# Optimization experiments

Measured on AMD Instinct MI355X. Metric: run time of the kernel, lower is better.

## Reference

```python
import jax, jax.numpy as jnp
import numpy as np

EPS = 1e-6  # AngularPhysicsConfig.eps


def setup_inputs() -> dict:
    key = jax.random.key(0)
    k1, k2 = jax.random.split(key)
    B, L, d, H = 2, 2048, 2048, 8
    x_spatial = jax.random.normal(k1, (B, L, d), dtype=jnp.float32)
    # attn is a softmax output: rows sum to 1 over the last axis
    attn = jax.nn.softmax(jax.random.normal(k2, (B, H, L, L), dtype=jnp.float32), axis=-1)
    W = jnp.ones((1,), dtype=jnp.float32)   # nn.Parameter(torch.ones(1))
    b = jnp.zeros((1,), dtype=jnp.float32)  # bias_init = 0.0
    return {"x_spatial": x_spatial, "attn": attn, "W": W, "b": b}


def reference(x_spatial, attn, W, b):
    # --- angular_kernel ---
    norm = jnp.clip(jnp.linalg.norm(x_spatial, axis=-1, keepdims=True), EPS, None)
    x_unit = x_spatial / norm                                   # [B, L, d]
    K = jnp.einsum('bld,bmd->blm', x_unit, x_unit)              # [B, L, L] cosine sim
    K_mean = K.mean(axis=(-1, -2), keepdims=True)
    K_cent = K - K_mean
    # torch .std() is unbiased (ddof=1), computed on detached K_cent
    K_std = jnp.std(jax.lax.stop_gradient(K_cent), axis=(-1, -2), keepdims=True, ddof=1)
    K_norm = K_cent / jnp.clip(K_std, EPS, None)                # [B, L, L]

    # --- compute_cos_align (detach_attn_for_alignment=True) ---
    A = jax.lax.stop_gradient(attn.mean(axis=1))                # [B, L, L]
    cos_align = jnp.sum(A * K_norm, axis=-1)                    # [B, L]

    # --- gate ---
    gate = jax.nn.sigmoid(W * cos_align + b)                    # [B, L]
    return gate, cos_align, K_norm
```

## Files before the change

### kernel.cpp

```cpp
#include <hip/hip_runtime.h>
#include <hip/hip_bf16.h>

#define L_DIM 2048
#define D_DIM 2048
#define B_DIM 2
#define H_DIM 8
#define NT 16
#define NPAIR 136
#define NRED 512
#define NKT (D_DIM / 64)
#define EPSV 1e-6f

using bf16x8 = __attribute__((ext_vector_type(8))) __bf16;
using f32x4  = __attribute__((ext_vector_type(4))) float;
using f4     = __attribute__((ext_vector_type(4))) float;

__device__ inline void gload_lds16(const void* g, void* l) {
    __builtin_amdgcn_global_load_lds(
        (const __attribute__((address_space(1))) void*)g,
        (__attribute__((address_space(3))) void*)l, 16, 0, 0);
}

__device__ inline ushort f2bf(float f) {
    unsigned int u = __float_as_uint(f);
    unsigned int lsb = (u >> 16) & 1u;
    u += 0x7fffu + lsb;
    return (ushort)(u >> 16);
}
__device__ inline float bf2f(ushort u) {
    return __uint_as_float(((unsigned int)u) << 16);
}

__global__ __launch_bounds__(256) void k_normalize(const float* __restrict__ x,
                                                   ushort* __restrict__ xu,
                                                   double* __restrict__ sums) {
    const int row = blockIdx.x;
    const int t   = threadIdx.x;
    const float* xr = x + (size_t)row * D_DIM;
    f4 v0 = __builtin_nontemporal_load(((const f4*)xr) + t);
    f4 v1 = __builtin_nontemporal_load(((const f4*)xr) + t + 256);
    float ss = v0.x*v0.x + v0.y*v0.y + v0.z*v0.z + v0.w*v0.w
             + v1.x*v1.x + v1.y*v1.y + v1.z*v1.z + v1.w*v1.w;
    #pragma unroll
    for (int off = 32; off; off >>= 1) ss += __shfl_down(ss, off);
    __shared__ float red[4];
    __shared__ float s_inv;
    if ((t & 63) == 0) red[t >> 6] = ss;
    __syncthreads();
    if (t == 0) {
        float nrm = sqrtf(red[0] + red[1] + red[2] + red[3]);
        nrm = fmaxf(nrm, EPSV);
        s_inv = 1.0f / nrm;
        if (row == 0) { sums[0] = 0.0; sums[1] = 0.0; sums[2] = 0.0; sums[3] = 0.0; }
    }
    __syncthreads();
    const float inv = s_inv;
    ushort* xo = xu + (size_t)row * D_DIM;
    ushort4 o0, o1;
    o0.x = f2bf(v0.x * inv); o0.y = f2bf(v0.y * inv);
    o0.z = f2bf(v0.z * inv); o0.w = f2bf(v0.w * inv);
    o1.x = f2bf(v1.x * inv); o1.y = f2bf(v1.y * inv);
    o1.z = f2bf(v1.z * inv); o1.w = f2bf(v1.w * inv);
    ((ushort4*)xo)[t]       = o0;
    ((ushort4*)xo)[t + 256] = o1;
}

__global__ __launch_bounds__(256) void k_mixed(const ushort* __restrict__ Xu,
                                               const float* __restrict__ attn,
                                               ushort* __restrict__ K16,
                                               double* __restrict__ sums,
                                               ushort* __restrict__ Amean) {
    __shared__ __align__(16) ushort lds_a[128 * 64];
    __shared__ __align__(16) ushort lds_b[128 * 64];
    const int t = threadIdx.x;
    const int batch = blockIdx.z;

    if (blockIdx.x >= NPAIR) {
        const int rid = blockIdx.x - NPAIR;
        const float* ab = attn + (size_t)batch * H_DIM * L_DIM * L_DIM;
        ushort* am = Amean + (size_t)batch * L_DIM * L_DIM;
        int i = rid * 256 + t;
        #pragma unroll
        for (int j = 0; j < 8; ++j, i += NRED * 256) {
            float4 s = {0.f, 0.f, 0.f, 0.f};
            #pragma unroll
            for (int h = 0; h < H_DIM; ++h) {
                const f4 v = __builtin_nontemporal_load(
                    ((const f4*)(ab + (size_t)h * L_DIM * L_DIM)) + i);
                s.x += v.x; s.y += v.y; s.z += v.z; s.w += v.w;
            }
            ushort4 o;
            o.x = f2bf(s.x * 0.125f); o.y = f2bf(s.y * 0.125f);
            o.z = f2bf(s.z * 0.125f); o.w = f2bf(s.w * 0.125f);
            ((ushort4*)am)[i] = o;
        }
        return;
    }

    const int lane = t & 63;
    const int w    = t >> 6;
    const int wr   = w >> 1, wc = w & 1;
    int ti = 0, rem = blockIdx.x;
    while (rem >= NT - ti) { rem -= NT - ti; ++ti; }
    const int tj = ti + rem;
    const int bRow = ti * 128;
    const int bCol = tj * 128;
    const bool diag = (ti == tj);
    const ushort* Xb = Xu + (size_t)batch * L_DIM * D_DIM;

    const int srow8  = t >> 3;
    const int schunk = ((t & 7) ^ (srow8 & 7)) * 8;
    const ushort* gA = Xb + (size_t)(bRow + srow8) * D_DIM + schunk;
    const ushort* gB = Xb + (size_t)(bCol + srow8) * D_DIM + schunk;
    ushort* lA = lds_a + t * 8;
    ushort* lB = lds_b + t * 8;

    f32x4 acc[4][4] = {};
    const int frow = lane & 15;
    const int fk   = lane >> 4;

    for (int kt = 0; kt < NKT; ++kt) {
        __syncthreads();
        const size_t ko = (size_t)kt * 64;
        #pragma unroll
        for (int i = 0; i < 4; ++i) {
            gload_lds16(gA + ko + (size_t)i * 32 * D_DIM, lA + i * 2048);
            gload_lds16(gB + ko + (size_t)i * 32 * D_DIM, lB + i * 2048);
        }
        __syncthreads();
        #pragma unroll
        for (int ks = 0; ks < 2; ++ks) {
            bf16x8 a[4], b[4];
            #pragma unroll
            for (int m = 0; m < 4; ++m) {
                const int R = wr * 64 + m * 16 + frow;
                a[m] = *(const bf16x8*)&lds_a[R * 64 + (((ks << 2) + fk) ^ (R & 7)) * 8];
            }
            #pragma unroll
            for (int n = 0; n < 4; ++n) {
                const int S = wc * 64 + n * 16 + frow;
                b[n] = *(const bf16x8*)&lds_b[S * 64 + (((ks << 2) + fk) ^ (S & 7)) * 8];
            }
            #pragma unroll
            for (int m = 0; m < 4; ++m)
                #pragma unroll
                for (int n = 0; n < 4; ++n)
                    acc[m][n] = __builtin_amdgcn_mfma_f32_16x16x32_bf16(a[m], b[n], acc[m][n], 0, 0, 0);
        }
    }

    ushort* Kb = K16 + (size_t)batch * L_DIM * L_DIM;
    float ps = 0.f, pss = 0.f;
    #pragma unroll
    for (int m = 0; m < 4; ++m) {
        #pragma unroll
        for (int n = 0; n < 4; ++n) {
            #pragma unroll
            for (int j = 0; j < 4; ++j) {
                const int r = bRow + wr * 64 + m * 16 + fk * 4 + j;
                const int c = bCol + wc * 64 + n * 16 + frow;
                const float v = acc[m][n][j];
                Kb[(size_t)r * L_DIM + c] = f2bf(v);
                ps += v; pss += v * v;
            }
            if (!diag) {
                const int rr  = bCol + wc * 64 + n * 16 + frow;
                const int cc0 = bRow + wr * 64 + m * 16 + fk * 4;
                ushort4 mq;
                mq.x = f2bf(acc[m][n][0]); mq.y = f2bf(acc[m][n][1]);
                mq.z = f2bf(acc[m][n][2]); mq.w = f2bf(acc[m][n][3]);
                *(ushort4*)&Kb[(size_t)rr * L_DIM + cc0] = mq;
            }
        }
    }
    if (!diag) { ps *= 2.f; pss *= 2.f; }
    #pragma unroll
    for (int off = 32; off; off >>= 1) {
        ps  += __shfl_down(ps, off);
        pss += __shfl_down(pss, off);
    }
    __shared__ float redS[4], redSS[4];
    if (lane == 0) { redS[w] = ps; redSS[w] = pss; }
    __syncthreads();
    if (t == 0) {
        atomicAdd(&sums[batch * 2],     (double)(redS[0] + redS[1] + redS[2] + redS[3]));
        atomicAdd(&sums[batch * 2 + 1], (double)(redSS[0] + redSS[1] + redSS[2] + redSS[3]));
    }
}

__global__ __launch_bounds__(256) void k_epilogue(float* __restrict__ out,
                                                  const ushort* __restrict__ K16,
                                                  const ushort* __restrict__ Amean,
                                                  const double* __restrict__ sums,
                                                  const float* __restrict__ Wp,
                                                  const float* __restrict__ bp) {
    const int row = blockIdx.x;
    const int b = row >> 11;
    const int t = threadIdx.x;

    const double N = (double)L_DIM * (double)L_DIM;
    const double mean_d = sums[b * 2] / N;
    double var = (sums[b * 2 + 1] - N * mean_d * mean_d) / (N - 1.0);
    var = var > 0.0 ? var : 0.0;
    float sd = (float)sqrt(var);
    sd = fmaxf(sd, EPSV);
    const float inv_std = 1.0f / sd;
    const float mean = (float)mean_d;

    const ushort* krow = K16 + (size_t)row * L_DIM;
    const ushort* arow = Amean + (size_t)row * L_DIM;
    float* onrm = out + 2 * B_DIM * L_DIM + (size_t)row * L_DIM;

    const ushort4 k0 = ((const ushort4*)krow)[t * 2];
    const ushort4 k1 = ((const ushort4*)krow)[t * 2 + 1];
    const ushort4 a0 = ((const ushort4*)arow)[t * 2];
    const ushort4 a1 = ((const ushort4*)arow)[t * 2 + 1];
    float kf[8] = { bf2f(k0.x), bf2f(k0.y), bf2f(k0.z), bf2f(k0.w),
                    bf2f(k1.x), bf2f(k1.y), bf2f(k1.z), bf2f(k1.w) };
    float af[8] = { bf2f(a0.x), bf2f(a0.y), bf2f(a0.z), bf2f(a0.w),
                    bf2f(a1.x), bf2f(a1.y), bf2f(a1.z), bf2f(a1.w) };
    float dot = 0.f;
    #pragma unroll
    for (int j = 0; j < 8; ++j) dot += af[j] * kf[j];
    f4 n0, n1;
    n0.x = (kf[0] - mean) * inv_std; n0.y = (kf[1] - mean) * inv_std;
    n0.z = (kf[2] - mean) * inv_std; n0.w = (kf[3] - mean) * inv_std;
    n1.x = (kf[4] - mean) * inv_std; n1.y = (kf[5] - mean) * inv_std;
    n1.z = (kf[6] - mean) * inv_std; n1.w = (kf[7] - mean) * inv_std;
    __builtin_nontemporal_store(n0, ((f4*)onrm) + t * 2);
    __builtin_nontemporal_store(n1, ((f4*)onrm) + t * 2 + 1);

    #pragma unroll
    for (int off = 32; off; off >>= 1) dot += __shfl_down(dot, off);
    __shared__ float red[4];
    if ((t & 63) == 0) red[t >> 6] = dot;
    __syncthreads();
    if (t == 0) {
        const float dotv = red[0] + red[1] + red[2] + red[3];
        const float ca = (dotv - mean) * inv_std;
        out[B_DIM * L_DIM + row] = ca;
        const float z = Wp[0] * ca + bp[0];
        out[row] = 1.0f / (1.0f + expf(-z));
    }
}

extern "C" void kernel_launch(void* const* d_in, const int* in_sizes, int n_in,
                              void* d_out, int out_size, void* d_ws, size_t ws_size,
                              hipStream_t stream) {
    const float* x    = (const float*)d_in[0];
    const float* attn = (const float*)d_in[1];
    const float* W    = (const float*)d_in[2];
    const float* bb   = (const float*)d_in[3];
    float* out = (float*)d_out;

    const size_t MAT = (size_t)B_DIM * L_DIM * L_DIM;
    ushort* xu    = (ushort*)d_ws;
    double* sums  = (double*)((char*)d_ws + MAT * 2);
    ushort* Amean = (ushort*)((char*)d_ws + MAT * 2 + 256);
    ushort* K16   = (ushort*)((char*)d_ws + MAT * 4 + 256);

    hipLaunchKernelGGL(k_normalize, dim3(B_DIM * L_DIM), dim3(256), 0, stream,
                       x, xu, sums);
    hipLaunchKernelGGL(k_mixed, dim3(NPAIR + NRED, 1, B_DIM), dim3(256), 0, stream,
                       xu, attn, K16, sums, Amean);
    hipLaunchKernelGGL(k_epilogue, dim3(B_DIM * L_DIM), dim3(256), 0, stream,
                       out, K16, Amean, sums, W, bb);
}
```

Baseline: 106.1 us.

## Load GEMM fragments directly from global memory instead of staging through LDS

The GEMM tiles in the mixed kernel no longer stage through LDS with global_load_lds and two barriers per k-step. Each wave now loads its bf16 MFMA fragments straight from global memory (relying on L2/L1 for reuse across waves) and loops over 32-wide k-steps without synchronisation. It also raises occupancy via launch_bounds(256,4) and renames the reduction block count constant. This removes barrier stalls and LDS traffic, but each element is now fetched by multiple waves from cache with strided 16-byte row accesses, which may raise global/L2 load pressure.

```diff
diff --git a/kernel.cpp b/kernel.cpp
--- a/kernel.cpp
+++ b/kernel.cpp
@@ -8,18 +8,12 @@
 #define NT 16
 #define NPAIR 136
 #define NRED 512
-#define NKT (D_DIM / 64)
+#define NSTREAM 512
 #define EPSV 1e-6f
 
 using bf16x8 = __attribute__((ext_vector_type(8))) __bf16;
 using f32x4  = __attribute__((ext_vector_type(4))) float;
 using f4     = __attribute__((ext_vector_type(4))) float;
-
-__device__ inline void gload_lds16(const void* g, void* l) {
-    __builtin_amdgcn_global_load_lds(
-        (const __attribute__((address_space(1))) void*)g,
-        (__attribute__((address_space(3))) void*)l, 16, 0, 0);
-}
 
 __device__ inline ushort f2bf(float f) {
     unsigned int u = __float_as_uint(f);
@@ -65,13 +59,11 @@
     ((ushort4*)xo)[t + 256] = o1;
 }
 
-__global__ __launch_bounds__(256) void k_mixed(const ushort* __restrict__ Xu,
-                                               const float* __restrict__ attn,
-                                               ushort* __restrict__ K16,
-                                               double* __restrict__ sums,
-                                               ushort* __restrict__ Amean) {
-    __shared__ __align__(16) ushort lds_a[128 * 64];
-    __shared__ __align__(16) ushort lds_b[128 * 64];
+__global__ __launch_bounds__(256, 4) void k_mixed(const ushort* __restrict__ Xu,
+                                                  const float* __restrict__ attn,
+                                                  ushort* __restrict__ K16,
+                                                  double* __restrict__ sums,
+                                                  ushort* __restrict__ Amean) {
     const int t = threadIdx.x;
     const int batch = blockIdx.z;
 
@@ -108,45 +100,28 @@
     const bool diag = (ti == tj);
     const ushort* Xb = Xu + (size_t)batch * L_DIM * D_DIM;
 
-    const int srow8  = t >> 3;
-    const int schunk = ((t & 7) ^ (srow8 & 7)) * 8;
-    const ushort* gA = Xb + (size_t)(bRow + srow8) * D_DIM + schunk;
-    const ushort* gB = Xb + (size_t)(bCol + srow8) * D_DIM + schunk;
-    ushort* lA = lds_a + t * 8;
-    ushort* lB = lds_b + t * 8;
-
-    f32x4 acc[4][4] = {};
     const int frow = lane & 15;
     const int fk   = lane >> 4;
-
-    for (int kt = 0; kt < NKT; ++kt) {
-        __syncthreads();
-        const size_t ko = (size_t)kt * 64;
-        #pragma unroll
-        for (int i = 0; i < 4; ++i) {
-            gload_lds16(gA + ko + (size_t)i * 32 * D_DIM, lA + i * 2048);
-            gload_lds16(gB + ko + (size_t)i * 32 * D_DIM, lB + i * 2048);
-        }
-        __syncthreads();
-        #pragma unroll
-        for (int ks = 0; ks < 2; ++ks) {
-            bf16x8 a[4], b[4];
+    const ushort* pA = Xb + (size_t)(bRow + wr * 64 + frow) * D_DIM + fk * 8;
+    const ushort* pB = Xb + (size_t)(bCol + wc * 64 + frow) * D_DIM + fk * 8;
+
+    f32x4 acc[4][4] = {};
+
+    #pragma unroll 2
+    for (int kt = 0; kt < D_DIM / 32; ++kt) {
+        const int ko = kt * 32;
+        bf16x8 a[4], b[4];
+        #pragma unroll
+        for (int m = 0; m < 4; ++m)
+            a[m] = *(const bf16x8*)(pA + (size_t)m * 16 * D_DIM + ko);
+        #pragma unroll
+        for (int n = 0; n < 4; ++n)
+            b[n] = *(const bf16x8*)(pB + (size_t)n * 16 * D_DIM + ko);
+        #pragma unroll
+        for (int m = 0; m < 4; ++m)
             #pragma unroll
-            for (int m = 0; m < 4; ++m) {
-                const int R = wr * 64 + m * 16 + frow;
-                a[m] = *(const bf16x8*)&lds_a[R * 64 + (((ks << 2) + fk) ^ (R & 7)) * 8];
-            }
-            #pragma unroll
-            for (int n = 0; n < 4; ++n) {
-                const int S = wc * 64 + n * 16 + frow;
-                b[n] = *(const bf16x8*)&lds_b[S * 64 + (((ks << 2) + fk) ^ (S & 7)) * 8];
-            }
-            #pragma unroll
-            for (int m = 0; m < 4; ++m)
-                #pragma unroll
-                for (int n = 0; n < 4; ++n)
-                    acc[m][n] = __builtin_amdgcn_mfma_f32_16x16x32_bf16(a[m], b[n], acc[m][n], 0, 0, 0);
-        }
+            for (int n = 0; n < 4; ++n)
+                acc[m][n] = __builtin_amdgcn_mfma_f32_16x16x32_bf16(a[m], b[n], acc[m][n], 0, 0, 0);
     }
 
     ushort* Kb = K16 + (size_t)batch * L_DIM * L_DIM;
@@ -261,7 +236,7 @@
 
     hipLaunchKernelGGL(k_normalize, dim3(B_DIM * L_DIM), dim3(256), 0, stream,
                        x, xu, sums);
-    hipLaunchKernelGGL(k_mixed, dim3(NPAIR + NRED, 1, B_DIM), dim3(256), 0, stream,
+    hipLaunchKernelGGL(k_mixed, dim3(NPAIR + NSTREAM, 1, B_DIM), dim3(256), 0, stream,
                        xu, attn, K16, sums, Amean);
     hipLaunchKernelGGL(k_epilogue, dim3(B_DIM * L_DIM), dim3(256), 0, stream,
                        out, K16, Amean, sums, W, bb);
```

New measurement: 191.4 us. +80.4%, slower.
